# Performance work log

Measured on AMD Instinct MI355X. Metric: run time of the kernel, lower is better.

The kernel has to match this reference:

```python
import jax, jax.numpy as jnp
import numpy as np


def setup_inputs() -> dict:
    key = jax.random.key(0)
    ks = jax.random.split(key, 8)
    B, S, F, K, E, N = 20000, 10, 128, 16, 128, 200000
    nodes = jax.random.randint(ks[0], (B,), 0, N)
    neigh_idx = jax.random.randint(ks[1], (B, S), 0, N)
    self_table = jax.random.normal(ks[2], (N, F), dtype=jnp.float32)
    neigh_table = jax.random.normal(ks[3], (N, F), dtype=jnp.float32)
    center = jax.random.normal(ks[4], (K, F), dtype=jnp.float32)
    cluster_mask = jax.random.uniform(ks[5], (K, F), dtype=jnp.float32)
    # xavier-like scaling keeps exp(relu(.)) in a sane range
    weight = jax.random.normal(ks[6], (E, 2 * F), dtype=jnp.float32) * 0.05
    alpha = jax.random.normal(ks[7], (2 * F, 1), dtype=jnp.float32) * 0.05
    return {"nodes": nodes, "neigh_idx": neigh_idx, "self_table": self_table,
            "neigh_table": neigh_table, "center": center, "cluster_mask": cluster_mask,
            "weight": weight, "alpha": alpha}


def reference(nodes, neigh_idx, self_table, neigh_table, center, cluster_mask, weight, alpha):
    B, S = neigh_idx.shape
    F = self_table.shape[1]
    self_feat = self_table[nodes]                       # (B, F)
    neigh = neigh_table[neigh_idx]                      # (B, S, F) gather (== mask.matmul in original)
    # attention over sampled neighbors: exp(relu([self || neigh] @ alpha))
    a_self, a_neigh = alpha[:F, 0], alpha[F:, 0]        # split cat-matmul
    logits = self_feat @ a_self                         # (B,)
    logits = logits[:, None] + neigh @ a_neigh          # (B, S)
    att = jnp.exp(jax.nn.relu(logits))
    att_norm = att / jnp.sum(att, axis=1, keepdims=True)
    # inverse-distance soft assignment to k centers (Student-t, degree 1)
    n2 = jnp.sum(neigh * neigh, axis=-1)                # (B, S)
    c2 = jnp.sum(center * center, axis=-1)              # (K,)
    cross = jnp.einsum('bsf,kf->bsk', neigh, center)    # (B, S, K)
    q = 1.0 / (n2[:, :, None] - 2.0 * cross + c2[None, None, :] + 1.0)  # (B, S, K)
    # clustered features: sum_k q[b,s,k] * mask[k,f] * neigh[b,s,f]
    clustered = neigh * jnp.einsum('bsk,kf->bsf', q, cluster_mask)      # (B, S, F)
    neigh_agg = jnp.sum(clustered * att_norm[:, :, None], axis=1)       # (B, F)
    combined = jnp.concatenate([self_feat, neigh_agg], axis=1)          # (B, 2F)
    return jax.nn.relu(combined @ weight.T)                             # (B, E)
```

## Files before the change

### kernel.cpp

```cpp
#include <hip/hip_runtime.h>
#include <hip/hip_bf16.h>

typedef unsigned short ushort_t;
typedef __attribute__((ext_vector_type(4))) float v4f;
typedef __attribute__((ext_vector_type(8))) short v8s;

#define FDIM 128
#define KCLUST 16
#define CSTRIDE 264
#define QSTRIDE 24

__device__ __forceinline__ ushort_t f2bf(float x) {
    unsigned int u = __float_as_uint(x);
    unsigned int r = (u + 0x7fffu + ((u >> 16) & 1u)) >> 16;
    return (ushort_t)r;
}
__device__ __forceinline__ float bf2f(ushort_t h) {
    return __uint_as_float((unsigned int)h << 16);
}

union V8U { v8s v; ushort_t u[8]; };

__global__ void pack_weight(const float* __restrict__ W, ushort_t* __restrict__ Wb,
                            long total, long valid) {
    long i = ((long)blockIdx.x * blockDim.x + threadIdx.x) * 4;
    if (i >= total) return;
    float4 v;
    if (i < valid) v = *(const float4*)(W + i);
    else           v = make_float4(0.f, 0.f, 0.f, 0.f);
    ushort_t* dst = Wb + i;
    dst[0] = f2bf(v.x); dst[1] = f2bf(v.y); dst[2] = f2bf(v.z); dst[3] = f2bf(v.w);
}

__global__ __launch_bounds__(512, 2) void fused_agg(
    const int* __restrict__ nodes, const int* __restrict__ neigh_idx,
    const float* __restrict__ self_table, const float* __restrict__ neigh_table,
    const float* __restrict__ center, const float* __restrict__ cluster_mask,
    const float* __restrict__ alpha, const ushort_t* __restrict__ Wb,
    float* __restrict__ out, int B, int S, int E) {

    __shared__ __align__(16) ushort_t comb[16 * CSTRIDE];
    __shared__ __align__(16) ushort_t nbf[2][16 * 128];
    __shared__ __align__(16) float    nf32[2][16 * 132];
    __shared__ __align__(16) float    attL[2][16];
    __shared__ __align__(16) float    n2L[2][16];
    __shared__ __align__(16) ushort_t qhi[16 * QSTRIDE];
    __shared__ __align__(16) ushort_t qlo[16 * QSTRIDE];
    __shared__ __align__(16) float    invL[16];

    const int t    = threadIdx.x;
    const int lane = t & 63, wave = t >> 6;
    const int row  = t >> 5;
    const int fq   = t & 31;
    const int f0   = fq << 2;
    const int l16  = lane & 15, quad = lane >> 4;

    const int b0 = blockIdx.x * 16;
    int b = b0 + row; if (b >= B) b = B - 1;

    const float4 aS = *(const float4*)(alpha + f0);
    const float4 aN = *(const float4*)(alpha + FDIM + f0);

    float ls;
    {
        size_t node = (size_t)nodes[b];
        float4 sf = *(const float4*)(self_table + node * FDIM + f0);
        ushort_t h0 = f2bf(sf.x), h1 = f2bf(sf.y), h2 = f2bf(sf.z), h3 = f2bf(sf.w);
        uint2 pk;
        pk.x = (unsigned)h0 | ((unsigned)h1 << 16);
        pk.y = (unsigned)h2 | ((unsigned)h3 << 16);
        *(uint2*)(comb + row * CSTRIDE + f0) = pk;
        ls = sf.x * aS.x + sf.y * aS.y + sf.z * aS.z + sf.w * aS.w;
        #pragma unroll
        for (int off = 1; off <= 16; off <<= 1) ls += __shfl_xor(ls, off, 64);
    }

    v8s cbf[4]; float c2v = 0.f;
    if (wave == 0) {
        const float* crow = center + l16 * FDIM;
        #pragma unroll
        for (int kk = 0; kk < 4; kk++) {
            const float* p = crow + kk * 32 + quad * 8;
            float4 x = *(const float4*)p;
            float4 y = *(const float4*)(p + 4);
            V8U pk;
            pk.u[0] = f2bf(x.x); pk.u[1] = f2bf(x.y); pk.u[2] = f2bf(x.z); pk.u[3] = f2bf(x.w);
            pk.u[4] = f2bf(y.x); pk.u[5] = f2bf(y.y); pk.u[6] = f2bf(y.z); pk.u[7] = f2bf(y.w);
            cbf[kk] = pk.v;
            c2v += x.x*x.x + x.y*x.y + x.z*x.z + x.w*x.w
                 + y.x*y.x + y.y*y.y + y.z*y.z + y.w*y.w;
        }
        c2v += __shfl_xor(c2v, 16, 64);
        c2v += __shfl_xor(c2v, 32, 64);
    }

    v8s mhi, mlo;
    {
        V8U ph, pl;
        const int fcol = wave * 16 + l16;
        #pragma unroll
        for (int j = 0; j < 8; j++) {
            float mv = (quad < 2) ? cluster_mask[(quad * 8 + j) * FDIM + fcol] : 0.f;
            ushort_t h = f2bf(mv);
            ph.u[j] = h;
            pl.u[j] = f2bf(mv - bf2f(h));
        }
        mhi = ph.v; mlo = pl.v;
    }

    int idx0 = neigh_idx[(size_t)b * S];
    float4 n4 = *(const float4*)(neigh_table + (size_t)idx0 * FDIM + f0);
    int idx_next = (S > 1) ? neigh_idx[(size_t)b * S + 1] : 0;

    float attsum = 0.f;
    float acc0 = 0.f, acc1 = 0.f, acc2 = 0.f, acc3 = 0.f;

    for (int s = 0; s < S; s++) {
        const int buf = s & 1;
        const float4 cur = n4;
        if (s + 1 < S) {
            n4 = *(const float4*)(neigh_table + (size_t)idx_next * FDIM + f0);
            if (s + 2 < S) idx_next = neigh_idx[(size_t)b * S + s + 2];
        }

        *(float4*)(nf32[buf] + row * 132 + f0) = cur;
        {
            ushort_t h0 = f2bf(cur.x), h1 = f2bf(cur.y), h2 = f2bf(cur.z), h3 = f2bf(cur.w);
            uint2 pk;
            pk.x = (unsigned)h0 | ((unsigned)h1 << 16);
            pk.y = (unsigned)h2 | ((unsigned)h3 << 16);
            const int slot = (fq >> 1) ^ (row & 15);
            *(uint2*)((char*)(nbf[buf]) + row * 256 + slot * 16 + (fq & 1) * 8) = pk;
        }
        float pn = cur.x * aN.x + cur.y * aN.y + cur.z * aN.z + cur.w * aN.w;
        float p2 = cur.x * cur.x + cur.y * cur.y + cur.z * cur.z + cur.w * cur.w;
        #pragma unroll
        for (int off = 1; off <= 16; off <<= 1) {
            pn += __shfl_xor(pn, off, 64);
            p2 += __shfl_xor(p2, off, 64);
        }
        const float att = __expf(fmaxf(ls + pn, 0.f));
        attsum += att;
        if (fq == 0) { attL[buf][row] = att; n2L[buf][row] = p2; }

        asm volatile("s_waitcnt lgkmcnt(0)" ::: "memory");
        __builtin_amdgcn_s_barrier();
        asm volatile("" ::: "memory");

        if (wave == 0) {
            v4f xacc = {0.f, 0.f, 0.f, 0.f};
            #pragma unroll
            for (int kk = 0; kk < 4; kk++) {
                const int sl = (kk * 4 + quad) ^ l16;
                v8s af = *(const v8s*)((char*)(nbf[buf]) + l16 * 256 + sl * 16);
                xacc = __builtin_amdgcn_mfma_f32_16x16x32_bf16(af, cbf[kk], xacc, 0, 0, 0);
            }
            const float4 n2r = *(const float4*)(&n2L[buf][quad * 4]);
            #pragma unroll
            for (int r = 0; r < 4; r++) {
                const float n2v = (r == 0) ? n2r.x : (r == 1) ? n2r.y : (r == 2) ? n2r.z : n2r.w;
                const float d  = n2v - 2.f * xacc[r] + c2v;
                const float qv = 1.f / (d + 1.f);
                const ushort_t h = f2bf(qv);
                qhi[(quad * 4 + r) * QSTRIDE + l16] = h;
                qlo[(quad * 4 + r) * QSTRIDE + l16] = f2bf(qv - bf2f(h));
            }
        }

        asm volatile("s_waitcnt lgkmcnt(0)" ::: "memory");
        __builtin_amdgcn_s_barrier();
        asm volatile("" ::: "memory");

        v8s aqh = *(const v8s*)(qhi + l16 * QSTRIDE + (quad & 1) * 8);
        v8s aql = *(const v8s*)(qlo + l16 * QSTRIDE + (quad & 1) * 8);
        v4f mac = {0.f, 0.f, 0.f, 0.f};
        mac = __builtin_amdgcn_mfma_f32_16x16x32_bf16(aqh, mhi, mac, 0, 0, 0);
        mac = __builtin_amdgcn_mfma_f32_16x16x32_bf16(aql, mhi, mac, 0, 0, 0);
        mac = __builtin_amdgcn_mfma_f32_16x16x32_bf16(aqh, mlo, mac, 0, 0, 0);

        const float4 attr = *(const float4*)(&attL[buf][quad * 4]);
        const float* nfp = nf32[buf] + wave * 16 + l16;
        acc0 = fmaf(attr.x * mac[0], nfp[(quad * 4 + 0) * 132], acc0);
        acc1 = fmaf(attr.y * mac[1], nfp[(quad * 4 + 1) * 132], acc1);
        acc2 = fmaf(attr.z * mac[2], nfp[(quad * 4 + 2) * 132], acc2);
        acc3 = fmaf(attr.w * mac[3], nfp[(quad * 4 + 3) * 132], acc3);
    }

    if (fq == 0) invL[row] = 1.f / attsum;
    __syncthreads();
    {
        const float4 invr = *(const float4*)(&invL[quad * 4]);
        ushort_t* cp = comb + 128 + wave * 16 + l16;
        cp[(quad * 4 + 0) * CSTRIDE] = f2bf(acc0 * invr.x);
        cp[(quad * 4 + 1) * CSTRIDE] = f2bf(acc1 * invr.y);
        cp[(quad * 4 + 2) * CSTRIDE] = f2bf(acc2 * invr.z);
        cp[(quad * 4 + 3) * CSTRIDE] = f2bf(acc3 * invr.w);
    }

    const int Ntiles = (E + 15) >> 4;

    v8s bfr[8];
    {
        const int nt0 = (wave < Ntiles) ? wave : 0;
        const ushort_t* wrow = Wb + (size_t)(nt0 * 16 + l16) * 256 + quad * 8;
        #pragma unroll
        for (int kk = 0; kk < 8; kk++)
            bfr[kk] = *(const v8s*)(wrow + kk * 32);
    }

    __syncthreads();

    v8s afr[8];
    #pragma unroll
    for (int kk = 0; kk < 8; kk++)
        afr[kk] = *(const v8s*)(comb + l16 * CSTRIDE + kk * 32 + quad * 8);

    for (int nt = wave; nt < Ntiles; nt += 8) {
        if (nt != wave) {
            const ushort_t* wrow = Wb + (size_t)(nt * 16 + l16) * 256 + quad * 8;
            #pragma unroll
            for (int kk = 0; kk < 8; kk++)
                bfr[kk] = *(const v8s*)(wrow + kk * 32);
        }
        v4f acc = {0.f, 0.f, 0.f, 0.f};
        #pragma unroll
        for (int kk = 0; kk < 8; kk++)
            acc = __builtin_amdgcn_mfma_f32_16x16x32_bf16(afr[kk], bfr[kk], acc, 0, 0, 0);
        const int gcol = nt * 16 + l16;
        if (gcol < E) {
            #pragma unroll
            for (int rr = 0; rr < 4; rr++) {
                const int grow = b0 + quad * 4 + rr;
                if (grow < B)
                    out[(size_t)grow * E + gcol] = fmaxf(acc[rr], 0.f);
            }
        }
    }
}

extern "C" void kernel_launch(void* const* d_in, const int* in_sizes, int n_in,
                              void* d_out, int out_size, void* d_ws, size_t ws_size,
                              hipStream_t stream) {
    const int*   nodes        = (const int*)d_in[0];
    const int*   neigh_idx    = (const int*)d_in[1];
    const float* self_table   = (const float*)d_in[2];
    const float* neigh_table  = (const float*)d_in[3];
    const float* center       = (const float*)d_in[4];
    const float* cluster_mask = (const float*)d_in[5];
    const float* weight       = (const float*)d_in[6];
    const float* alpha        = (const float*)d_in[7];
    float* out = (float*)d_out;

    int B = in_sizes[0];
    int S = in_sizes[1] / B;
    int E = in_sizes[6] / (2 * FDIM);

    int Np = ((E + 15) / 16) * 16;
    ushort_t* Wb = (ushort_t*)d_ws;

    long totalW = (long)Np * 256;
    long validW = (long)E * 256;
    int blksW = (int)((totalW + 1023) / 1024);
    pack_weight<<<blksW, 256, 0, stream>>>(weight, Wb, totalW, validW);

    int nblk = (B + 15) / 16;
    fused_agg<<<nblk, 512, 0, stream>>>(
        nodes, neigh_idx, self_table, neigh_table, center, cluster_mask, alpha,
        Wb, out, B, S, E);
}
```

Baseline: 232.3 us.

## Shrink tile to 8 rows per 256-thread block with two feature tiles per wave

Each block now handles 8 batch rows with 4 waves instead of 16 rows with 8 waves. Each wave covers two 16-column feature tiles in the cluster-mask MFMA stage and strides the output GEMM by 4 tiles. The 16-row MFMA shapes are kept, so half the rows are padding: duplicated rows via l16&7 with stores masked to quad<2. The goal is more resident blocks and shorter per-block barrier latency. The cost is wasted MFMA work, because half of every 16x16 tile is redundant, plus twice as many weight-tile loads per batch row.

```diff
diff --git a/kernel.cpp b/kernel.cpp
--- a/kernel.cpp
+++ b/kernel.cpp
@@ -32,21 +32,21 @@
     dst[0] = f2bf(v.x); dst[1] = f2bf(v.y); dst[2] = f2bf(v.z); dst[3] = f2bf(v.w);
 }
 
-__global__ __launch_bounds__(512, 2) void fused_agg(
+__global__ __launch_bounds__(256, 6) void fused_agg(
     const int* __restrict__ nodes, const int* __restrict__ neigh_idx,
     const float* __restrict__ self_table, const float* __restrict__ neigh_table,
     const float* __restrict__ center, const float* __restrict__ cluster_mask,
     const float* __restrict__ alpha, const ushort_t* __restrict__ Wb,
     float* __restrict__ out, int B, int S, int E) {
 
-    __shared__ __align__(16) ushort_t comb[16 * CSTRIDE];
-    __shared__ __align__(16) ushort_t nbf[2][16 * 128];
-    __shared__ __align__(16) float    nf32[2][16 * 132];
-    __shared__ __align__(16) float    attL[2][16];
-    __shared__ __align__(16) float    n2L[2][16];
-    __shared__ __align__(16) ushort_t qhi[16 * QSTRIDE];
-    __shared__ __align__(16) ushort_t qlo[16 * QSTRIDE];
-    __shared__ __align__(16) float    invL[16];
+    __shared__ __align__(16) ushort_t comb[8 * CSTRIDE];
+    __shared__ __align__(16) ushort_t nbf[2][8 * 128];
+    __shared__ __align__(16) float    nf32[2][8 * 132];
+    __shared__ __align__(16) float    attL[2][8];
+    __shared__ __align__(16) float    n2L[2][8];
+    __shared__ __align__(16) ushort_t qhi[8 * QSTRIDE];
+    __shared__ __align__(16) ushort_t qlo[8 * QSTRIDE];
+    __shared__ __align__(16) float    invL[8];
 
     const int t    = threadIdx.x;
     const int lane = t & 63, wave = t >> 6;
@@ -55,7 +55,7 @@
     const int f0   = fq << 2;
     const int l16  = lane & 15, quad = lane >> 4;
 
-    const int b0 = blockIdx.x * 16;
+    const int b0 = blockIdx.x * 8;
     int b = b0 + row; if (b >= B) b = B - 1;
 
     const float4 aS = *(const float4*)(alpha + f0);
@@ -94,18 +94,23 @@
         c2v += __shfl_xor(c2v, 32, 64);
     }
 
-    v8s mhi, mlo;
+    v8s mhi0, mlo0, mhi1, mlo1;
     {
         V8U ph, pl;
-        const int fcol = wave * 16 + l16;
         #pragma unroll
         for (int j = 0; j < 8; j++) {
-            float mv = (quad < 2) ? cluster_mask[(quad * 8 + j) * FDIM + fcol] : 0.f;
+            float mv = (quad < 2) ? cluster_mask[(quad * 8 + j) * FDIM + (wave * 2) * 16 + l16] : 0.f;
             ushort_t h = f2bf(mv);
-            ph.u[j] = h;
-            pl.u[j] = f2bf(mv - bf2f(h));
-        }
-        mhi = ph.v; mlo = pl.v;
+            ph.u[j] = h; pl.u[j] = f2bf(mv - bf2f(h));
+        }
+        mhi0 = ph.v; mlo0 = pl.v;
+        #pragma unroll
+        for (int j = 0; j < 8; j++) {
+            float mv = (quad < 2) ? cluster_mask[(quad * 8 + j) * FDIM + (wave * 2 + 1) * 16 + l16] : 0.f;
+            ushort_t h = f2bf(mv);
+            ph.u[j] = h; pl.u[j] = f2bf(mv - bf2f(h));
+        }
+        mhi1 = ph.v; mlo1 = pl.v;
     }
 
     int idx0 = neigh_idx[(size_t)b * S];
@@ -113,7 +118,8 @@
     int idx_next = (S > 1) ? neigh_idx[(size_t)b * S + 1] : 0;
 
     float attsum = 0.f;
-    float acc0 = 0.f, acc1 = 0.f, acc2 = 0.f, acc3 = 0.f;
+    float accA0 = 0.f, accA1 = 0.f, accA2 = 0.f, accA3 = 0.f;
+    float accB0 = 0.f, accB1 = 0.f, accB2 = 0.f, accB3 = 0.f;
 
     for (int s = 0; s < S; s++) {
         const int buf = s & 1;
@@ -129,7 +135,7 @@
             uint2 pk;
             pk.x = (unsigned)h0 | ((unsigned)h1 << 16);
             pk.y = (unsigned)h2 | ((unsigned)h3 << 16);
-            const int slot = (fq >> 1) ^ (row & 15);
+            const int slot = (fq >> 1) ^ row;
             *(uint2*)((char*)(nbf[buf]) + row * 256 + slot * 16 + (fq & 1) * 8) = pk;
         }
         float pn = cur.x * aN.x + cur.y * aN.y + cur.z * aN.z + cur.w * aN.w;
@@ -151,19 +157,22 @@
             v4f xacc = {0.f, 0.f, 0.f, 0.f};
             #pragma unroll
             for (int kk = 0; kk < 4; kk++) {
-                const int sl = (kk * 4 + quad) ^ l16;
-                v8s af = *(const v8s*)((char*)(nbf[buf]) + l16 * 256 + sl * 16);
+                const int r = l16 & 7;
+                const int sl = (kk * 4 + quad) ^ r;
+                v8s af = *(const v8s*)((char*)(nbf[buf]) + r * 256 + sl * 16);
                 xacc = __builtin_amdgcn_mfma_f32_16x16x32_bf16(af, cbf[kk], xacc, 0, 0, 0);
             }
-            const float4 n2r = *(const float4*)(&n2L[buf][quad * 4]);
-            #pragma unroll
-            for (int r = 0; r < 4; r++) {
-                const float n2v = (r == 0) ? n2r.x : (r == 1) ? n2r.y : (r == 2) ? n2r.z : n2r.w;
-                const float d  = n2v - 2.f * xacc[r] + c2v;
-                const float qv = 1.f / (d + 1.f);
-                const ushort_t h = f2bf(qv);
-                qhi[(quad * 4 + r) * QSTRIDE + l16] = h;
-                qlo[(quad * 4 + r) * QSTRIDE + l16] = f2bf(qv - bf2f(h));
+            if (quad < 2) {
+                const float4 n2r = *(const float4*)(&n2L[buf][quad * 4]);
+                #pragma unroll
+                for (int r = 0; r < 4; r++) {
+                    const float n2v = (r == 0) ? n2r.x : (r == 1) ? n2r.y : (r == 2) ? n2r.z : n2r.w;
+                    const float d  = n2v - 2.f * xacc[r] + c2v;
+                    const float qv = 1.f / (d + 1.f);
+                    const ushort_t h = f2bf(qv);
+                    qhi[(quad * 4 + r) * QSTRIDE + l16] = h;
+                    qlo[(quad * 4 + r) * QSTRIDE + l16] = f2bf(qv - bf2f(h));
+                }
             }
         }
 
@@ -171,30 +180,48 @@
         __builtin_amdgcn_s_barrier();
         asm volatile("" ::: "memory");
 
-        v8s aqh = *(const v8s*)(qhi + l16 * QSTRIDE + (quad & 1) * 8);
-        v8s aql = *(const v8s*)(qlo + l16 * QSTRIDE + (quad & 1) * 8);
-        v4f mac = {0.f, 0.f, 0.f, 0.f};
-        mac = __builtin_amdgcn_mfma_f32_16x16x32_bf16(aqh, mhi, mac, 0, 0, 0);
-        mac = __builtin_amdgcn_mfma_f32_16x16x32_bf16(aql, mhi, mac, 0, 0, 0);
-        mac = __builtin_amdgcn_mfma_f32_16x16x32_bf16(aqh, mlo, mac, 0, 0, 0);
-
-        const float4 attr = *(const float4*)(&attL[buf][quad * 4]);
-        const float* nfp = nf32[buf] + wave * 16 + l16;
-        acc0 = fmaf(attr.x * mac[0], nfp[(quad * 4 + 0) * 132], acc0);
-        acc1 = fmaf(attr.y * mac[1], nfp[(quad * 4 + 1) * 132], acc1);
-        acc2 = fmaf(attr.z * mac[2], nfp[(quad * 4 + 2) * 132], acc2);
-        acc3 = fmaf(attr.w * mac[3], nfp[(quad * 4 + 3) * 132], acc3);
+        v8s aqh = *(const v8s*)(qhi + (l16 & 7) * QSTRIDE + (quad & 1) * 8);
+        v8s aql = *(const v8s*)(qlo + (l16 & 7) * QSTRIDE + (quad & 1) * 8);
+        const float4 attr = *(const float4*)(&attL[buf][(quad & 1) * 4]);
+
+        v4f macA = {0.f, 0.f, 0.f, 0.f};
+        macA = __builtin_amdgcn_mfma_f32_16x16x32_bf16(aqh, mhi0, macA, 0, 0, 0);
+        macA = __builtin_amdgcn_mfma_f32_16x16x32_bf16(aql, mhi0, macA, 0, 0, 0);
+        macA = __builtin_amdgcn_mfma_f32_16x16x32_bf16(aqh, mlo0, macA, 0, 0, 0);
+        {
+            const float* nfp = nf32[buf] + (wave * 2) * 16 + l16;
+            accA0 = fmaf(attr.x * macA[0], nfp[(((quad & 1) * 4) + 0) * 132], accA0);
+            accA1 = fmaf(attr.y * macA[1], nfp[(((quad & 1) * 4) + 1) * 132], accA1);
+            accA2 = fmaf(attr.z * macA[2], nfp[(((quad & 1) * 4) + 2) * 132], accA2);
+            accA3 = fmaf(attr.w * macA[3], nfp[(((quad & 1) * 4) + 3) * 132], accA3);
+        }
+        v4f macB = {0.f, 0.f, 0.f, 0.f};
+        macB = __builtin_amdgcn_mfma_f32_16x16x32_bf16(aqh, mhi1, macB, 0, 0, 0);
+        macB = __builtin_amdgcn_mfma_f32_16x16x32_bf16(aql, mhi1, macB, 0, 0, 0);
+        macB = __builtin_amdgcn_mfma_f32_16x16x32_bf16(aqh, mlo1, macB, 0, 0, 0);
+        {
+            const float* nfp = nf32[buf] + (wave * 2 + 1) * 16 + l16;
+            accB0 = fmaf(attr.x * macB[0], nfp[(((quad & 1) * 4) + 0) * 132], accB0);
+            accB1 = fmaf(attr.y * macB[1], nfp[(((quad & 1) * 4) + 1) * 132], accB1);
+            accB2 = fmaf(attr.z * macB[2], nfp[(((quad & 1) * 4) + 2) * 132], accB2);
+            accB3 = fmaf(attr.w * macB[3], nfp[(((quad & 1) * 4) + 3) * 132], accB3);
+        }
     }
 
     if (fq == 0) invL[row] = 1.f / attsum;
     __syncthreads();
-    {
+    if (quad < 2) {
         const float4 invr = *(const float4*)(&invL[quad * 4]);
-        ushort_t* cp = comb + 128 + wave * 16 + l16;
-        cp[(quad * 4 + 0) * CSTRIDE] = f2bf(acc0 * invr.x);
-        cp[(quad * 4 + 1) * CSTRIDE] = f2bf(acc1 * invr.y);
-        cp[(quad * 4 + 2) * CSTRIDE] = f2bf(acc2 * invr.z);
-        cp[(quad * 4 + 3) * CSTRIDE] = f2bf(acc3 * invr.w);
+        ushort_t* cpA = comb + 128 + (wave * 2) * 16 + l16;
+        cpA[(quad * 4 + 0) * CSTRIDE] = f2bf(accA0 * invr.x);
+        cpA[(quad * 4 + 1) * CSTRIDE] = f2bf(accA1 * invr.y);
+        cpA[(quad * 4 + 2) * CSTRIDE] = f2bf(accA2 * invr.z);
+        cpA[(quad * 4 + 3) * CSTRIDE] = f2bf(accA3 * invr.w);
+        ushort_t* cpB = comb + 128 + (wave * 2 + 1) * 16 + l16;
+        cpB[(quad * 4 + 0) * CSTRIDE] = f2bf(accB0 * invr.x);
+        cpB[(quad * 4 + 1) * CSTRIDE] = f2bf(accB1 * invr.y);
+        cpB[(quad * 4 + 2) * CSTRIDE] = f2bf(accB2 * invr.z);
+        cpB[(quad * 4 + 3) * CSTRIDE] = f2bf(accB3 * invr.w);
     }
 
     const int Ntiles = (E + 15) >> 4;
@@ -213,9 +240,9 @@
     v8s afr[8];
     #pragma unroll
     for (int kk = 0; kk < 8; kk++)
-        afr[kk] = *(const v8s*)(comb + l16 * CSTRIDE + kk * 32 + quad * 8);
-
-    for (int nt = wave; nt < Ntiles; nt += 8) {
+        afr[kk] = *(const v8s*)(comb + (l16 & 7) * CSTRIDE + kk * 32 + quad * 8);
+
+    for (int nt = wave; nt < Ntiles; nt += 4) {
         if (nt != wave) {
             const ushort_t* wrow = Wb + (size_t)(nt * 16 + l16) * 256 + quad * 8;
             #pragma unroll
@@ -227,7 +254,7 @@
         for (int kk = 0; kk < 8; kk++)
             acc = __builtin_amdgcn_mfma_f32_16x16x32_bf16(afr[kk], bfr[kk], acc, 0, 0, 0);
         const int gcol = nt * 16 + l16;
-        if (gcol < E) {
+        if (gcol < E && quad < 2) {
             #pragma unroll
             for (int rr = 0; rr < 4; rr++) {
                 const int grow = b0 + quad * 4 + rr;
@@ -263,8 +290,8 @@
     int blksW = (int)((totalW + 1023) / 1024);
     pack_weight<<<blksW, 256, 0, stream>>>(weight, Wb, totalW, validW);
 
-    int nblk = (B + 15) / 16;
-    fused_agg<<<nblk, 512, 0, stream>>>(
+    int nblk = (B + 7) / 8;
+    fused_agg<<<nblk, 256, 0, stream>>>(
         nodes, neigh_idx, self_table, neigh_table, center, cluster_mask, alpha,
         Wb, out, B, S, E);
 }
```

Result: slower. 301.7 us (+29.9%).

## Specialize for S=10: gather all neighbors upfront, batch cluster MFMAs across waves

Applied to the files above, without the earlier changes.

For S equal to 10 the kernel now loads all ten neighbor rows at once into LDS instead of walking a serial per-neighbor loop with two barriers each. The distance MFMAs are spread over 8 waves, one neighbor per wave, rather than running on wave 0 alone. The fp32 neighbor values for the final weighting are re-gathered from global memory into registers rather than kept in LDS. This removes about 20 block barriers and the single-wave bottleneck, at the cost of more LDS and registers, a second global gather, and a slow generic fallback kernel for other S.

```diff
diff --git a/kernel.cpp b/kernel.cpp
--- a/kernel.cpp
+++ b/kernel.cpp
@@ -9,6 +9,7 @@
 #define KCLUST 16
 #define CSTRIDE 264
 #define QSTRIDE 24
+#define SS 10
 
 __device__ __forceinline__ ushort_t f2bf(float x) {
     unsigned int u = __float_as_uint(x);
@@ -17,6 +18,11 @@
 }
 __device__ __forceinline__ float bf2f(ushort_t h) {
     return __uint_as_float((unsigned int)h << 16);
+}
+__device__ __forceinline__ float wave_reduce_sum(float v) {
+    #pragma unroll
+    for (int off = 32; off > 0; off >>= 1) v += __shfl_xor(v, off, 64);
+    return v;
 }
 
 union V8U { v8s v; ushort_t u[8]; };
@@ -32,51 +38,50 @@
     dst[0] = f2bf(v.x); dst[1] = f2bf(v.y); dst[2] = f2bf(v.z); dst[3] = f2bf(v.w);
 }
 
-__global__ __launch_bounds__(512, 2) void fused_agg(
+__global__ __launch_bounds__(512, 2) void fused_agg_s10(
     const int* __restrict__ nodes, const int* __restrict__ neigh_idx,
     const float* __restrict__ self_table, const float* __restrict__ neigh_table,
     const float* __restrict__ center, const float* __restrict__ cluster_mask,
     const float* __restrict__ alpha, const ushort_t* __restrict__ Wb,
-    float* __restrict__ out, int B, int S, int E) {
+    float* __restrict__ out, int B, int E) {
 
     __shared__ __align__(16) ushort_t comb[16 * CSTRIDE];
-    __shared__ __align__(16) ushort_t nbf[2][16 * 128];
-    __shared__ __align__(16) float    nf32[2][16 * 132];
-    __shared__ __align__(16) float    attL[2][16];
-    __shared__ __align__(16) float    n2L[2][16];
-    __shared__ __align__(16) ushort_t qhi[16 * QSTRIDE];
-    __shared__ __align__(16) ushort_t qlo[16 * QSTRIDE];
-    __shared__ __align__(16) float    invL[16];
+    __shared__ __align__(16) ushort_t nbf[SS * 16 * 128];
+    __shared__ __align__(16) ushort_t qhi[SS * 16 * QSTRIDE];
+    __shared__ __align__(16) ushort_t qlo[SS * 16 * QSTRIDE];
+    __shared__ __align__(16) float    attL[SS * 16];
+    __shared__ __align__(16) float    n2L[SS * 16];
+    __shared__ __align__(16) int      idxL[SS * 16];
 
     const int t    = threadIdx.x;
     const int lane = t & 63, wave = t >> 6;
-    const int row  = t >> 5;
+    const int g    = t >> 5;
     const int fq   = t & 31;
     const int f0   = fq << 2;
     const int l16  = lane & 15, quad = lane >> 4;
 
     const int b0 = blockIdx.x * 16;
-    int b = b0 + row; if (b >= B) b = B - 1;
+    int bg = b0 + g; if (bg >= B) bg = B - 1;
 
     const float4 aS = *(const float4*)(alpha + f0);
     const float4 aN = *(const float4*)(alpha + FDIM + f0);
 
     float ls;
     {
-        size_t node = (size_t)nodes[b];
+        size_t node = (size_t)nodes[bg];
         float4 sf = *(const float4*)(self_table + node * FDIM + f0);
         ushort_t h0 = f2bf(sf.x), h1 = f2bf(sf.y), h2 = f2bf(sf.z), h3 = f2bf(sf.w);
         uint2 pk;
         pk.x = (unsigned)h0 | ((unsigned)h1 << 16);
         pk.y = (unsigned)h2 | ((unsigned)h3 << 16);
-        *(uint2*)(comb + row * CSTRIDE + f0) = pk;
+        *(uint2*)(comb + g * CSTRIDE + f0) = pk;
         ls = sf.x * aS.x + sf.y * aS.y + sf.z * aS.z + sf.w * aS.w;
         #pragma unroll
         for (int off = 1; off <= 16; off <<= 1) ls += __shfl_xor(ls, off, 64);
     }
 
     v8s cbf[4]; float c2v = 0.f;
-    if (wave == 0) {
+    {
         const float* crow = center + l16 * FDIM;
         #pragma unroll
         for (int kk = 0; kk < 4; kk++) {
@@ -97,40 +102,34 @@
     v8s mhi, mlo;
     {
         V8U ph, pl;
-        const int fcol = wave * 16 + l16;
+        const int fc = wave * 16 + l16;
         #pragma unroll
         for (int j = 0; j < 8; j++) {
-            float mv = (quad < 2) ? cluster_mask[(quad * 8 + j) * FDIM + fcol] : 0.f;
+            float mv = (quad < 2) ? cluster_mask[(quad * 8 + j) * FDIM + fc] : 0.f;
             ushort_t h = f2bf(mv);
-            ph.u[j] = h;
-            pl.u[j] = f2bf(mv - bf2f(h));
+            ph.u[j] = h; pl.u[j] = f2bf(mv - bf2f(h));
         }
         mhi = ph.v; mlo = pl.v;
     }
 
-    int idx0 = neigh_idx[(size_t)b * S];
-    float4 n4 = *(const float4*)(neigh_table + (size_t)idx0 * FDIM + f0);
-    int idx_next = (S > 1) ? neigh_idx[(size_t)b * S + 1] : 0;
-
-    float attsum = 0.f;
-    float acc0 = 0.f, acc1 = 0.f, acc2 = 0.f, acc3 = 0.f;
-
-    for (int s = 0; s < S; s++) {
-        const int buf = s & 1;
-        const float4 cur = n4;
-        if (s + 1 < S) {
-            n4 = *(const float4*)(neigh_table + (size_t)idx_next * FDIM + f0);
-            if (s + 2 < S) idx_next = neigh_idx[(size_t)b * S + s + 2];
-        }
-
-        *(float4*)(nf32[buf] + row * 132 + f0) = cur;
+    int idxv[SS];
+    #pragma unroll
+    for (int j = 0; j < SS; j++) idxv[j] = neigh_idx[(size_t)bg * SS + j];
+    if (fq == 0) {
+        #pragma unroll
+        for (int j = 0; j < SS; j++) idxL[j * 16 + g] = idxv[j];
+    }
+
+    #pragma unroll
+    for (int j = 0; j < SS; j++) {
+        const float4 cur = *(const float4*)(neigh_table + (size_t)idxv[j] * FDIM + f0);
         {
             ushort_t h0 = f2bf(cur.x), h1 = f2bf(cur.y), h2 = f2bf(cur.z), h3 = f2bf(cur.w);
             uint2 pk;
             pk.x = (unsigned)h0 | ((unsigned)h1 << 16);
             pk.y = (unsigned)h2 | ((unsigned)h3 << 16);
-            const int slot = (fq >> 1) ^ (row & 15);
-            *(uint2*)((char*)(nbf[buf]) + row * 256 + slot * 16 + (fq & 1) * 8) = pk;
+            const int slot = (fq >> 1) ^ g;
+            *(uint2*)((char*)nbf + (j * 16 + g) * 256 + slot * 16 + (fq & 1) * 8) = pk;
         }
         float pn = cur.x * aN.x + cur.y * aN.y + cur.z * aN.z + cur.w * aN.w;
         float p2 = cur.x * cur.x + cur.y * cur.y + cur.z * cur.z + cur.w * cur.w;
@@ -140,61 +139,70 @@
             p2 += __shfl_xor(p2, off, 64);
         }
         const float att = __expf(fmaxf(ls + pn, 0.f));
-        attsum += att;
-        if (fq == 0) { attL[buf][row] = att; n2L[buf][row] = p2; }
-
-        asm volatile("s_waitcnt lgkmcnt(0)" ::: "memory");
-        __builtin_amdgcn_s_barrier();
-        asm volatile("" ::: "memory");
-
-        if (wave == 0) {
-            v4f xacc = {0.f, 0.f, 0.f, 0.f};
-            #pragma unroll
-            for (int kk = 0; kk < 4; kk++) {
-                const int sl = (kk * 4 + quad) ^ l16;
-                v8s af = *(const v8s*)((char*)(nbf[buf]) + l16 * 256 + sl * 16);
-                xacc = __builtin_amdgcn_mfma_f32_16x16x32_bf16(af, cbf[kk], xacc, 0, 0, 0);
-            }
-            const float4 n2r = *(const float4*)(&n2L[buf][quad * 4]);
-            #pragma unroll
-            for (int r = 0; r < 4; r++) {
-                const float n2v = (r == 0) ? n2r.x : (r == 1) ? n2r.y : (r == 2) ? n2r.z : n2r.w;
-                const float d  = n2v - 2.f * xacc[r] + c2v;
-                const float qv = 1.f / (d + 1.f);
-                const ushort_t h = f2bf(qv);
-                qhi[(quad * 4 + r) * QSTRIDE + l16] = h;
-                qlo[(quad * 4 + r) * QSTRIDE + l16] = f2bf(qv - bf2f(h));
-            }
-        }
-
-        asm volatile("s_waitcnt lgkmcnt(0)" ::: "memory");
-        __builtin_amdgcn_s_barrier();
-        asm volatile("" ::: "memory");
-
-        v8s aqh = *(const v8s*)(qhi + l16 * QSTRIDE + (quad & 1) * 8);
-        v8s aql = *(const v8s*)(qlo + l16 * QSTRIDE + (quad & 1) * 8);
+        if (fq == 0) { attL[j * 16 + g] = att; n2L[j * 16 + g] = p2; }
+    }
+
+    asm volatile("s_waitcnt lgkmcnt(0)" ::: "memory");
+    __builtin_amdgcn_s_barrier();
+    asm volatile("" ::: "memory");
+
+    const int fcol = wave * 16 + l16;
+    float nReg[SS * 4];
+    #pragma unroll
+    for (int s = 0; s < SS; s++) {
+        const int4 iv = *(const int4*)&idxL[s * 16 + quad * 4];
+        nReg[s * 4 + 0] = neigh_table[(size_t)iv.x * FDIM + fcol];
+        nReg[s * 4 + 1] = neigh_table[(size_t)iv.y * FDIM + fcol];
+        nReg[s * 4 + 2] = neigh_table[(size_t)iv.z * FDIM + fcol];
+        nReg[s * 4 + 3] = neigh_table[(size_t)iv.w * FDIM + fcol];
+    }
+
+    for (int s = wave; s < SS; s += 8) {
+        v4f xacc = {0.f, 0.f, 0.f, 0.f};
+        #pragma unroll
+        for (int kk = 0; kk < 4; kk++) {
+            const int sl = (kk * 4 + quad) ^ l16;
+            v8s af = *(const v8s*)((const char*)nbf + (s * 16 + l16) * 256 + sl * 16);
+            xacc = __builtin_amdgcn_mfma_f32_16x16x32_bf16(af, cbf[kk], xacc, 0, 0, 0);
+        }
+        const float4 n2r = *(const float4*)&n2L[s * 16 + quad * 4];
+        #pragma unroll
+        for (int r = 0; r < 4; r++) {
+            const float n2v = (r == 0) ? n2r.x : (r == 1) ? n2r.y : (r == 2) ? n2r.z : n2r.w;
+            const float d  = n2v - 2.f * xacc[r] + c2v;
+            const float qv = 1.f / (d + 1.f);
+            const ushort_t h = f2bf(qv);
+            qhi[(s * 16 + quad * 4 + r) * QSTRIDE + l16] = h;
+            qlo[(s * 16 + quad * 4 + r) * QSTRIDE + l16] = f2bf(qv - bf2f(h));
+        }
+    }
+
+    asm volatile("s_waitcnt lgkmcnt(0)" ::: "memory");
+    __builtin_amdgcn_s_barrier();
+    asm volatile("" ::: "memory");
+
+    float a0 = 0.f, a1 = 0.f, a2 = 0.f, a3 = 0.f;
+    float t0 = 0.f, t1 = 0.f, t2 = 0.f, t3 = 0.f;
+    #pragma unroll
+    for (int s = 0; s < SS; s++) {
+        v8s aqh = *(const v8s*)(qhi + (s * 16 + l16) * QSTRIDE + (quad & 1) * 8);
+        v8s aql = *(const v8s*)(qlo + (s * 16 + l16) * QSTRIDE + (quad & 1) * 8);
         v4f mac = {0.f, 0.f, 0.f, 0.f};
         mac = __builtin_amdgcn_mfma_f32_16x16x32_bf16(aqh, mhi, mac, 0, 0, 0);
         mac = __builtin_amdgcn_mfma_f32_16x16x32_bf16(aql, mhi, mac, 0, 0, 0);
         mac = __builtin_amdgcn_mfma_f32_16x16x32_bf16(aqh, mlo, mac, 0, 0, 0);
-
-        const float4 attr = *(const float4*)(&attL[buf][quad * 4]);
-        const float* nfp = nf32[buf] + wave * 16 + l16;
-        acc0 = fmaf(attr.x * mac[0], nfp[(quad * 4 + 0) * 132], acc0);
-        acc1 = fmaf(attr.y * mac[1], nfp[(quad * 4 + 1) * 132], acc1);
-        acc2 = fmaf(attr.z * mac[2], nfp[(quad * 4 + 2) * 132], acc2);
-        acc3 = fmaf(attr.w * mac[3], nfp[(quad * 4 + 3) * 132], acc3);
-    }
-
-    if (fq == 0) invL[row] = 1.f / attsum;
-    __syncthreads();
-    {
-        const float4 invr = *(const float4*)(&invL[quad * 4]);
-        ushort_t* cp = comb + 128 + wave * 16 + l16;
-        cp[(quad * 4 + 0) * CSTRIDE] = f2bf(acc0 * invr.x);
-        cp[(quad * 4 + 1) * CSTRIDE] = f2bf(acc1 * invr.y);
-        cp[(quad * 4 + 2) * CSTRIDE] = f2bf(acc2 * invr.z);
-        cp[(quad * 4 + 3) * CSTRIDE] = f2bf(acc3 * invr.w);
+        const float4 attq = *(const float4*)&attL[s * 16 + quad * 4];
+        a0 = fmaf(attq.x * mac[0], nReg[s * 4 + 0], a0); t0 += attq.x;
+        a1 = fmaf(attq.y * mac[1], nReg[s * 4 + 1], a1); t1 += attq.y;
+        a2 = fmaf(attq.z * mac[2], nReg[s * 4 + 2], a2); t2 += attq.z;
+        a3 = fmaf(attq.w * mac[3], nReg[s * 4 + 3], a3); t3 += attq.w;
+    }
+    {
+        ushort_t* cp = comb + 128 + fcol;
+        cp[(quad * 4 + 0) * CSTRIDE] = f2bf(a0 / t0);
+        cp[(quad * 4 + 1) * CSTRIDE] = f2bf(a1 / t1);
+        cp[(quad * 4 + 2) * CSTRIDE] = f2bf(a2 / t2);
+        cp[(quad * 4 + 3) * CSTRIDE] = f2bf(a3 / t3);
     }
 
     const int Ntiles = (E + 15) >> 4;
@@ -208,7 +216,9 @@
             bfr[kk] = *(const v8s*)(wrow + kk * 32);
     }
 
-    __syncthreads();
+    asm volatile("s_waitcnt lgkmcnt(0)" ::: "memory");
+    __builtin_amdgcn_s_barrier();
+    asm volatile("" ::: "memory");
 
     v8s afr[8];
     #pragma unroll
@@ -235,6 +245,51 @@
                     out[(size_t)grow * E + gcol] = fmaxf(acc[rr], 0.f);
             }
         }
+    }
+}
+
+__global__ void fused_generic(
+    const int* __restrict__ nodes, const int* __restrict__ neigh_idx,
+    const float* __restrict__ self_table, const float* __restrict__ neigh_table,
+    const float* __restrict__ center, const float* __restrict__ cluster_mask,
+    const float* __restrict__ alpha, const float* __restrict__ weight,
+    float* __restrict__ out, int B, int S, int E) {
+
+    __shared__ float combsh[256];
+    const int b = blockIdx.x;
+    const int lane = threadIdx.x;
+
+    float s0 = self_table[(size_t)nodes[b] * FDIM + lane];
+    float s1 = self_table[(size_t)nodes[b] * FDIM + 64 + lane];
+    const float ls = wave_reduce_sum(s0 * alpha[lane] + s1 * alpha[64 + lane]);
+
+    float acc0 = 0.f, acc1 = 0.f, attsum = 0.f;
+    for (int s = 0; s < S; s++) {
+        const size_t idx = (size_t)neigh_idx[(size_t)b * S + s];
+        const float n0 = neigh_table[idx * FDIM + lane];
+        const float n1 = neigh_table[idx * FDIM + 64 + lane];
+        const float ln = wave_reduce_sum(n0 * alpha[128 + lane] + n1 * alpha[192 + lane]);
+        const float att = __expf(fmaxf(ls + ln, 0.f));
+        float m0 = 0.f, m1 = 0.f;
+        for (int k = 0; k < KCLUST; k++) {
+            const float c0 = center[k * FDIM + lane];
+            const float c1 = center[k * FDIM + 64 + lane];
+            const float d = wave_reduce_sum((n0 - c0) * (n0 - c0) + (n1 - c1) * (n1 - c1));
+            const float qv = 1.f / (d + 1.f);
+            m0 += qv * cluster_mask[k * FDIM + lane];
+            m1 += qv * cluster_mask[k * FDIM + 64 + lane];
+        }
+        acc0 += att * n0 * m0; acc1 += att * n1 * m1; attsum += att;
+    }
+    const float inv = 1.f / attsum;
+    combsh[lane] = s0; combsh[64 + lane] = s1;
+    combsh[128 + lane] = acc0 * inv; combsh[192 + lane] = acc1 * inv;
+    __syncthreads();
+    for (int e = lane; e < E; e += 64) {
+        const float* wr = weight + (size_t)e * 256;
+        float o = 0.f;
+        for (int j = 0; j < 256; j++) o += combsh[j] * wr[j];
+        out[(size_t)b * E + e] = fmaxf(o, 0.f);
     }
 }
 
@@ -255,16 +310,21 @@
     int S = in_sizes[1] / B;
     int E = in_sizes[6] / (2 * FDIM);
 
-    int Np = ((E + 15) / 16) * 16;
-    ushort_t* Wb = (ushort_t*)d_ws;
-
-    long totalW = (long)Np * 256;
-    long validW = (long)E * 256;
-    int blksW = (int)((totalW + 1023) / 1024);
-    pack_weight<<<blksW, 256, 0, stream>>>(weight, Wb, totalW, validW);
-
-    int nblk = (B + 15) / 16;
-    fused_agg<<<nblk, 512, 0, stream>>>(
-        nodes, neigh_idx, self_table, neigh_table, center, cluster_mask, alpha,
-        Wb, out, B, S, E);
-}
+    if (S == SS) {
+        int Np = ((E + 15) / 16) * 16;
+        ushort_t* Wb = (ushort_t*)d_ws;
+        long totalW = (long)Np * 256;
+        long validW = (long)E * 256;
+        int blksW = (int)((totalW + 1023) / 1024);
+        pack_weight<<<blksW, 256, 0, stream>>>(weight, Wb, totalW, validW);
+
+        int nblk = (B + 15) / 16;
+        fused_agg_s10<<<nblk, 512, 0, stream>>>(
+            nodes, neigh_idx, self_table, neigh_table, center, cluster_mask,
+            alpha, Wb, out, B, E);
+    } else {
+        fused_generic<<<B, 64, 0, stream>>>(
+            nodes, neigh_idx, self_table, neigh_table, center, cluster_mask,
+            alpha, weight, out, B, S, E);
+    }
+}
```

Result: slower. 245.8 us (+5.8%).
